# Optimization experiments

Measured on AMD Instinct MI355X. Metric: run time of the kernel, lower is better.

## Reference

```python
import jax, jax.numpy as jnp
import numpy as np

QMIN, QMAX = -128.0, 127.0  # int8 range


def _fake_int_cast(t):
    # Emulates .to(torch.int8) on an already-clamped float tensor:
    # truncation toward zero, then back to float.
    return jnp.trunc(t)


def setup_inputs() -> dict:
    key = jax.random.key(0)
    k_x, k_w, k_ws, k_is, k_b = jax.random.split(key, 5)
    B, S, IN, OUT = 4, 2048, 4096, 4096
    x = jax.random.normal(k_x, (B, S, IN), dtype=jnp.float32)
    # quant_weight buffer holds int8 values (stored here as fp32 integers),
    # produced by quantizing a dense fp weight with per-out-channel scales.
    weight_scale = jax.random.uniform(k_ws, (OUT, 1), dtype=jnp.float32, minval=0.005, maxval=0.02)
    w_fp = jax.random.normal(k_w, (OUT, IN), dtype=jnp.float32) * 0.02
    quant_weight = jnp.trunc(jnp.clip(w_fp / weight_scale, QMIN, QMAX))
    input_scale = jax.random.uniform(k_is, (1,), dtype=jnp.float32, minval=0.01, maxval=0.03)
    bias = jax.random.normal(k_b, (OUT,), dtype=jnp.float32)
    return {"x": x, "quant_weight": quant_weight, "weight_scale": weight_scale,
            "input_scale": input_scale, "bias": bias}


def reference(x, quant_weight, weight_scale, input_scale, bias):
    # quantize input: clamp(x/scale) -> int8 (trunc toward zero) -> float
    quant_input = _fake_int_cast(jnp.clip(x / input_scale, QMIN, QMAX))
    # int8 matmul performed in fp32: [B,S,IN] @ [OUT,IN]^T -> [B,S,OUT]
    quant_output = jnp.einsum("bsi,oi->bso", quant_input, quant_weight)
    # dequantize with combined per-out-channel scale, viewed [1,1,OUT]
    scale = (weight_scale * input_scale).reshape((1,) * (quant_output.ndim - 1) + (-1,))
    output = quant_output * scale
    output = output + bias
    return output
```

## Files before the change

### kernel.cpp

```cpp
#include <hip/hip_runtime.h>


using v4i = __attribute__((ext_vector_type(4))) int;

typedef const __attribute__((address_space(1))) signed char gc_t;
typedef __attribute__((address_space(3))) signed char lc_t;

constexpr int BM = 128;
constexpr int BN = 128;
constexpr int BK = 128;


__device__ __forceinline__ int quant4(const float4 f, float s) {
    int a = (int)fminf(fmaxf(f.x / s, -128.0f), 127.0f);
    int b = (int)fminf(fmaxf(f.y / s, -128.0f), 127.0f);
    int c = (int)fminf(fmaxf(f.z / s, -128.0f), 127.0f);
    int d = (int)fminf(fmaxf(f.w / s, -128.0f), 127.0f);
    return (a & 0xff) | ((b & 0xff) << 8) | ((c & 0xff) << 16) | ((d & 0xff) << 24);
}

__global__ void quant_x_kernel(const float4* __restrict__ x,
                               const float* __restrict__ scale,
                               int* __restrict__ out, int n4) {
    const float s = scale[0];
    int i = blockIdx.x * blockDim.x + threadIdx.x;
    if (i >= n4) return;
    out[i] = quant4(x[i], s);
}

__global__ void quant_w_kernel(const float4* __restrict__ w,
                               int* __restrict__ out, int n4) {
    int i = blockIdx.x * blockDim.x + threadIdx.x;
    if (i >= n4) return;
    float4 f = w[i];
    out[i] = ((int)f.x & 0xff) | (((int)f.y & 0xff) << 8) |
             (((int)f.z & 0xff) << 16) | (((int)f.w & 0xff) << 24);
}


__global__ __launch_bounds__(256, 4) void gemm_i8_kernel(
    const signed char* __restrict__ Aq,
    const signed char* __restrict__ Wq,
    const float* __restrict__ wscale,
    const float* __restrict__ iscale,
    const float* __restrict__ bias,
    float* __restrict__ C,
    int M, int N, int K)
{
    __shared__ signed char As[BM * BK];
    __shared__ signed char Bs[BN * BK];

    const int tid  = threadIdx.x;
    const int wave = tid >> 6;
    const int lane = tid & 63;
    const int wm   = (wave >> 1) * 64;
    const int wn   = (wave & 1) * 64;

    const int m0 = blockIdx.y * BM;
    const int n0 = blockIdx.x * BN;

    const int srow = lane >> 3;
    const int gchunk = (lane & 7) ^ srow;

    const int fr = lane & 15;
    const int qh = lane >> 4;
    const int coff0 = (((0 * 4) + qh) ^ (fr & 7)) * 16;
    const int coff1 = (((1 * 4) + qh) ^ (fr & 7)) * 16;

    v4i acc[4][4];
#pragma unroll
    for (int i = 0; i < 4; ++i)
#pragma unroll
        for (int j = 0; j < 4; ++j) acc[i][j] = (v4i){0, 0, 0, 0};

    const size_t Kz = (size_t)K;
    const signed char* pA = Aq + (size_t)(m0 + wave * 32 + srow) * Kz + gchunk * 16;
    const signed char* pB = Wq + (size_t)(n0 + wave * 32 + srow) * Kz + gchunk * 16;
    lc_t* lA = (lc_t*)(As + (wave * 32) * BK);
    lc_t* lB = (lc_t*)(Bs + (wave * 32) * BK);

    for (int k0 = 0; k0 < K; k0 += BK) {
#pragma unroll
        for (int c = 0; c < 4; ++c) {
            __builtin_amdgcn_global_load_lds((gc_t*)(pA + (size_t)(c * 8) * Kz),
                                             lA + c * 8 * BK, 16, 0, 0);
            __builtin_amdgcn_global_load_lds((gc_t*)(pB + (size_t)(c * 8) * Kz),
                                             lB + c * 8 * BK, 16, 0, 0);
        }
        pA += BK;
        pB += BK;
        __syncthreads();

#pragma unroll
        for (int s = 0; s < 2; ++s) {
            const int coff = s ? coff1 : coff0;
            v4i af[4], bf[4];
#pragma unroll
            for (int t = 0; t < 4; ++t)
                af[t] = *(const v4i*)(As + (wm + t * 16 + fr) * BK + coff);
#pragma unroll
            for (int t = 0; t < 4; ++t)
                bf[t] = *(const v4i*)(Bs + (wn + t * 16 + fr) * BK + coff);
#pragma unroll
            for (int mt = 0; mt < 4; ++mt)
#pragma unroll
                for (int nt = 0; nt < 4; ++nt)
                    acc[mt][nt] = __builtin_amdgcn_mfma_i32_16x16x64_i8(
                        af[mt], bf[nt], acc[mt][nt], 0, 0, 0);
        }
        __syncthreads();
    }

    const float is = iscale[0];
#pragma unroll
    for (int nt = 0; nt < 4; ++nt) {
        const int col = n0 + wn + nt * 16 + fr;
        const float sc = wscale[col] * is;
        const float bv = bias[col];
#pragma unroll
        for (int mt = 0; mt < 4; ++mt) {
            const int rbase = m0 + wm + mt * 16 + qh * 4;
#pragma unroll
            for (int r = 0; r < 4; ++r) {
                C[(size_t)(rbase + r) * N + col] = (float)acc[mt][nt][r] * sc + bv;
            }
        }
    }
}


extern "C" void kernel_launch(void* const* d_in, const int* in_sizes, int n_in,
                              void* d_out, int out_size, void* d_ws, size_t ws_size,
                              hipStream_t stream) {
    const float* x  = (const float*)d_in[0];
    const float* qw = (const float*)d_in[1];
    const float* ws = (const float*)d_in[2];
    const float* is = (const float*)d_in[3];
    const float* bs = (const float*)d_in[4];
    float* out = (float*)d_out;

    const int nx = in_sizes[0];
    const int nw = in_sizes[1];
    const int N  = in_sizes[4];
    const int K  = nw / N;
    const int M  = nx / K;

    signed char* xq = (signed char*)d_ws;
    signed char* wq = (signed char*)d_ws + (size_t)nx;

    quant_x_kernel<<<nx / 4 / 256, 256, 0, stream>>>(
        (const float4*)x, is, (int*)xq, nx / 4);
    quant_w_kernel<<<nw / 4 / 256, 256, 0, stream>>>(
        (const float4*)qw, (int*)wq, nw / 4);

    dim3 grid(N / BN, M / BM);
    gemm_i8_kernel<<<grid, 256, 0, stream>>>(xq, wq, ws, is, bs, out, M, N, K);
}
```

Measured before the change: 378.1 us.

## Switch int8 GEMM to 32x32x32 MFMA and fuse quantization kernels

Replaces the 4x4 grid of 16x16x64 int8 MFMAs per wave with a 2x2 grid of 32x32x32 MFMAs. This changes the LDS fragment addressing and the epilogue row mapping, and halves the fragment loads per k-step. It also merges the x and weight quantization kernels into a single launch. The larger MFMA shape needs fewer LDS reads per FLOP, but it may change issue efficiency and makes the output stores less contiguous per lane.

```diff
diff --git a/kernel.cpp b/kernel.cpp
--- a/kernel.cpp
+++ b/kernel.cpp
@@ -1,7 +1,8 @@
 #include <hip/hip_runtime.h>
 
 
-using v4i = __attribute__((ext_vector_type(4))) int;
+using v4i  = __attribute__((ext_vector_type(4))) int;
+using v16i = __attribute__((ext_vector_type(16))) int;
 
 typedef const __attribute__((address_space(1))) signed char gc_t;
 typedef __attribute__((address_space(3))) signed char lc_t;
@@ -19,22 +20,23 @@
     return (a & 0xff) | ((b & 0xff) << 8) | ((c & 0xff) << 16) | ((d & 0xff) << 24);
 }
 
-__global__ void quant_x_kernel(const float4* __restrict__ x,
-                               const float* __restrict__ scale,
-                               int* __restrict__ out, int n4) {
-    const float s = scale[0];
+__global__ void quant_fused_kernel(const float4* __restrict__ x,
+                                   const float4* __restrict__ w,
+                                   const float* __restrict__ scale,
+                                   int* __restrict__ outx,
+                                   int* __restrict__ outw,
+                                   int nx4, int nw4) {
     int i = blockIdx.x * blockDim.x + threadIdx.x;
-    if (i >= n4) return;
-    out[i] = quant4(x[i], s);
-}
-
-__global__ void quant_w_kernel(const float4* __restrict__ w,
-                               int* __restrict__ out, int n4) {
-    int i = blockIdx.x * blockDim.x + threadIdx.x;
-    if (i >= n4) return;
-    float4 f = w[i];
-    out[i] = ((int)f.x & 0xff) | (((int)f.y & 0xff) << 8) |
-             (((int)f.z & 0xff) << 16) | (((int)f.w & 0xff) << 24);
+    if (i < nx4) {
+        outx[i] = quant4(x[i], scale[0]);
+    } else {
+        int j = i - nx4;
+        if (j < nw4) {
+            float4 f = w[j];
+            outw[j] = ((int)f.x & 0xff) | (((int)f.y & 0xff) << 8) |
+                      (((int)f.z & 0xff) << 16) | (((int)f.w & 0xff) << 24);
+        }
+    }
 }
 
 
@@ -59,19 +61,22 @@
     const int m0 = blockIdx.y * BM;
     const int n0 = blockIdx.x * BN;
 
-    const int srow = lane >> 3;
+    const int srow   = lane >> 3;
     const int gchunk = (lane & 7) ^ srow;
 
-    const int fr = lane & 15;
-    const int qh = lane >> 4;
-    const int coff0 = (((0 * 4) + qh) ^ (fr & 7)) * 16;
-    const int coff1 = (((1 * 4) + qh) ^ (fr & 7)) * 16;
+    const int fr = lane & 31;
+    const int kh = lane >> 5;
+    int coff[4];
+#pragma unroll
+    for (int s = 0; s < 4; ++s) coff[s] = ((s * 2 + kh) ^ (fr & 7)) * 16;
 
-    v4i acc[4][4];
+    v16i acc[2][2];
 #pragma unroll
-    for (int i = 0; i < 4; ++i)
+    for (int i = 0; i < 2; ++i)
 #pragma unroll
-        for (int j = 0; j < 4; ++j) acc[i][j] = (v4i){0, 0, 0, 0};
+        for (int j = 0; j < 2; ++j)
+#pragma unroll
+            for (int r = 0; r < 16; ++r) acc[i][j][r] = 0;
 
     const size_t Kz = (size_t)K;
     const signed char* pA = Aq + (size_t)(m0 + wave * 32 + srow) * Kz + gchunk * 16;
@@ -92,20 +97,19 @@
         __syncthreads();
 
 #pragma unroll
-        for (int s = 0; s < 2; ++s) {
-            const int coff = s ? coff1 : coff0;
-            v4i af[4], bf[4];
+        for (int s = 0; s < 4; ++s) {
+            v4i af[2], bf[2];
 #pragma unroll
-            for (int t = 0; t < 4; ++t)
-                af[t] = *(const v4i*)(As + (wm + t * 16 + fr) * BK + coff);
+            for (int t = 0; t < 2; ++t)
+                af[t] = *(const v4i*)(As + (wm + t * 32 + fr) * BK + coff[s]);
 #pragma unroll
-            for (int t = 0; t < 4; ++t)
-                bf[t] = *(const v4i*)(Bs + (wn + t * 16 + fr) * BK + coff);
+            for (int t = 0; t < 2; ++t)
+                bf[t] = *(const v4i*)(Bs + (wn + t * 32 + fr) * BK + coff[s]);
 #pragma unroll
-            for (int mt = 0; mt < 4; ++mt)
+            for (int mt = 0; mt < 2; ++mt)
 #pragma unroll
-                for (int nt = 0; nt < 4; ++nt)
-                    acc[mt][nt] = __builtin_amdgcn_mfma_i32_16x16x64_i8(
+                for (int nt = 0; nt < 2; ++nt)
+                    acc[mt][nt] = __builtin_amdgcn_mfma_i32_32x32x32_i8(
                         af[mt], bf[nt], acc[mt][nt], 0, 0, 0);
         }
         __syncthreads();
@@ -113,16 +117,17 @@
 
     const float is = iscale[0];
 #pragma unroll
-    for (int nt = 0; nt < 4; ++nt) {
-        const int col = n0 + wn + nt * 16 + fr;
+    for (int nt = 0; nt < 2; ++nt) {
+        const int col = n0 + wn + nt * 32 + fr;
         const float sc = wscale[col] * is;
         const float bv = bias[col];
 #pragma unroll
-        for (int mt = 0; mt < 4; ++mt) {
-            const int rbase = m0 + wm + mt * 16 + qh * 4;
+        for (int mt = 0; mt < 2; ++mt) {
+            const int rbase = m0 + wm + mt * 32 + 4 * kh;
 #pragma unroll
-            for (int r = 0; r < 4; ++r) {
-                C[(size_t)(rbase + r) * N + col] = (float)acc[mt][nt][r] * sc + bv;
+            for (int r = 0; r < 16; ++r) {
+                const int row = rbase + (r & 3) + 8 * (r >> 2);
+                C[(size_t)row * N + col] = (float)acc[mt][nt][r] * sc + bv;
             }
         }
     }
@@ -148,10 +153,10 @@
     signed char* xq = (signed char*)d_ws;
     signed char* wq = (signed char*)d_ws + (size_t)nx;
 
-    quant_x_kernel<<<nx / 4 / 256, 256, 0, stream>>>(
-        (const float4*)x, is, (int*)xq, nx / 4);
-    quant_w_kernel<<<nw / 4 / 256, 256, 0, stream>>>(
-        (const float4*)qw, (int*)wq, nw / 4);
+    const int nx4 = nx / 4, nw4 = nw / 4;
+    const int qblocks = (nx4 + nw4 + 255) / 256;
+    quant_fused_kernel<<<qblocks, 256, 0, stream>>>(
+        (const float4*)x, (const float4*)qw, is, (int*)xq, (int*)wq, nx4, nw4);
 
     dim3 grid(N / BN, M / BM);
     gemm_i8_kernel<<<grid, 256, 0, stream>>>(xq, wq, ws, is, bs, out, M, N, K);
```

New measurement: 390.8 us. 1.03x slower.
